# Kernel tuning notes

Hardware: AMD Instinct MI355X
Metric: run time of the kernel (lower is better)

Reference implementation:

```python
import jax, jax.numpy as jnp
import numpy as np

B = 512
DIM_X = 128
DIM_Y = 128
HIDDEN = 512


def setup_inputs() -> dict:
    key = jax.random.key(0)
    kx, ky, kw1, kw2 = jax.random.split(key, 4)
    x = jax.random.normal(kx, (B, DIM_X), dtype=jnp.float32)
    y = jax.random.normal(ky, (B, DIM_Y), dtype=jnp.float32)
    # Glorot-ish scaling for the Dense layers
    W1 = jax.random.normal(kw1, (DIM_X + DIM_Y, HIDDEN), dtype=jnp.float32) * (1.0 / np.sqrt(DIM_X + DIM_Y))
    b1 = jnp.zeros((HIDDEN,), dtype=jnp.float32)
    W2 = jax.random.normal(kw2, (HIDDEN, 1), dtype=jnp.float32) * (1.0 / np.sqrt(HIDDEN))
    b2 = jnp.zeros((1,), dtype=jnp.float32)
    return {"x": x, "y": y, "W1": W1, "b1": b1, "W2": W2, "b2": b2}


def reference(x, y, W1, b1, W2, b2):
    # scores[i, j] = f(concat(x_i, y_j)) with f = Dense(512, relu) -> Dense(1).
    # Since the first Dense is linear in the concatenated input, split W1 into
    # the x-block and y-block and broadcast-sum instead of materializing the
    # [B*B, dim_x+dim_y] concat tensor (same math as tile+concat+matmul).
    dim_x = x.shape[1]
    hx = x @ W1[:dim_x]          # [B, H]
    hy = y @ W1[dim_x:]          # [B, H]
    h = jax.nn.relu(hx[:, None, :] + hy[None, :, :] + b1)  # [B, B, H]
    scores = jnp.einsum('ijh,h->ij', h, W2[:, 0]) + b2[0]   # [B, B]
    return scores
```

## Files before the change

### kernel.cpp

```cpp
#include <hip/hip_runtime.h>


#define BATCH 512
#define DX    128
#define HID   512

typedef _Float16 half2_t __attribute__((ext_vector_type(2)));

static __device__ __forceinline__ half2_t u2h(unsigned int u) {
    union { unsigned int u; half2_t h; } c; c.u = u; return c.h;
}
static __device__ __forceinline__ unsigned int h2u(half2_t h) {
    union { half2_t h; unsigned int u; } c; c.h = h; return c.u;
}

__global__ __launch_bounds__(256) void proj_kernel(
    const float* __restrict__ x, const float* __restrict__ y,
    const float* __restrict__ W1, const float* __restrict__ b1,
    _Float16* __restrict__ hxy)
{
    const int part = blockIdx.y;
    const int row0 = blockIdx.x * 8;
    const int h0   = blockIdx.z * 256;
    const float* __restrict__ src = part ? y : x;
    const float* __restrict__ W   = W1 + part * DX * HID;

    __shared__ __align__(16) float s[8][DX];
    {
        const int t = threadIdx.x;
        const int r = t >> 5, c4 = (t & 31) << 2;
        *(float4*)&s[r][c4] = *(const float4*)&src[(row0 + r) * DX + c4];
    }
    __syncthreads();

    const int hthr = threadIdx.x & 63;
    const int rg   = threadIdx.x >> 6;
    const int h    = h0 + hthr * 4;
    const int ra   = rg * 2, rb = ra + 1;

    float a0 = 0.f, a1 = 0.f, a2 = 0.f, a3 = 0.f;
    float c0 = 0.f, c1 = 0.f, c2 = 0.f, c3 = 0.f;

    #pragma unroll 2
    for (int k4 = 0; k4 < DX / 4; ++k4) {
        const float4 xa = *(const float4*)&s[ra][k4 * 4];
        const float4 xb = *(const float4*)&s[rb][k4 * 4];
        #pragma unroll
        for (int kk = 0; kk < 4; ++kk) {
            const float4 wv = *(const float4*)&W[(k4 * 4 + kk) * HID + h];
            const float fa = (kk == 0) ? xa.x : (kk == 1) ? xa.y : (kk == 2) ? xa.z : xa.w;
            const float fb = (kk == 0) ? xb.x : (kk == 1) ? xb.y : (kk == 2) ? xb.z : xb.w;
            a0 = fmaf(fa, wv.x, a0); a1 = fmaf(fa, wv.y, a1);
            a2 = fmaf(fa, wv.z, a2); a3 = fmaf(fa, wv.w, a3);
            c0 = fmaf(fb, wv.x, c0); c1 = fmaf(fb, wv.y, c1);
            c2 = fmaf(fb, wv.z, c2); c3 = fmaf(fb, wv.w, c3);
        }
    }

    float4 bias = make_float4(0.f, 0.f, 0.f, 0.f);
    if (part) bias = *(const float4*)&b1[h];

    half2_t p0, p1;
    p0.x = (_Float16)(a0 + bias.x); p0.y = (_Float16)(a1 + bias.y);
    p1.x = (_Float16)(a2 + bias.z); p1.y = (_Float16)(a3 + bias.w);
    uint2 st0; st0.x = h2u(p0); st0.y = h2u(p1);
    *(uint2*)&hxy[(part * BATCH + row0 + ra) * HID + h] = st0;

    p0.x = (_Float16)(c0 + bias.x); p0.y = (_Float16)(c1 + bias.y);
    p1.x = (_Float16)(c2 + bias.z); p1.y = (_Float16)(c3 + bias.w);
    uint2 st1; st1.x = h2u(p0); st1.y = h2u(p1);
    *(uint2*)&hxy[(part * BATCH + row0 + rb) * HID + h] = st1;
}

#define TI   128
#define TJ   64
#define HPW  32
#define IST  132
#define JST  68

__global__ __launch_bounds__(512, 2) void score_kernel(
    const _Float16* __restrict__ hxy, const float* __restrict__ W2,
    unsigned int* __restrict__ pws16)
{
    __shared__ __align__(16) unsigned int sA[HPW * IST];
    __shared__ __align__(16) unsigned int sB[HPW * JST];
    __shared__ unsigned int sW[HPW];

    const int i0  = blockIdx.y * TI;
    const int j0  = blockIdx.x * TJ;
    const int z   = blockIdx.z;
    const int hp0 = z * HPW;
    const int tid = threadIdx.x;
    const unsigned int* __restrict__ hx32 = (const unsigned int*)hxy;

    #pragma unroll
    for (int it = 0; it < 2; ++it) {
        const int sidx = tid + it * 512;
        const int row = sidx >> 3, q = sidx & 7;
        const uint4 v = *(const uint4*)&hx32[(i0 + row) * 256 + hp0 + (q << 2)];
        unsigned int* p = &sA[(q << 2) * IST + row];
        p[0 * IST] = v.x; p[1 * IST] = v.y; p[2 * IST] = v.z; p[3 * IST] = v.w;
    }
    {
        const int row = tid >> 3, q = tid & 7;
        const uint4 v = *(const uint4*)&hx32[(BATCH + j0 + row) * 256 + hp0 + (q << 2)];
        unsigned int* p = &sB[(q << 2) * JST + row];
        p[0 * JST] = v.x; p[1 * JST] = v.y; p[2 * JST] = v.z; p[3 * JST] = v.w;
    }
    if (tid < HPW) {
        const float2 w = *(const float2*)&W2[2 * (hp0 + tid)];
        half2_t wh; wh.x = (_Float16)w.x; wh.y = (_Float16)w.y;
        sW[tid] = h2u(wh);
    }
    __syncthreads();

    const int tx = tid & 15;
    const int ty = tid >> 4;
    const unsigned int* pa = &sA[ty << 2];
    const unsigned int* pb = &sB[tx << 2];

    float acc[4][4] = {{0.f,0.f,0.f,0.f},{0.f,0.f,0.f,0.f},
                       {0.f,0.f,0.f,0.f},{0.f,0.f,0.f,0.f}};
    const half2_t hz = {(_Float16)0, (_Float16)0};

    #pragma unroll 4
    for (int hp = 0; hp < HPW; ++hp) {
        const half2_t w = u2h(sW[hp]);
        const uint4 av = *(const uint4*)&pa[hp * IST];
        const uint4 bv = *(const uint4*)&pb[hp * JST];
        half2_t a[4] = {u2h(av.x), u2h(av.y), u2h(av.z), u2h(av.w)};
        half2_t b[4] = {u2h(bv.x), u2h(bv.y), u2h(bv.z), u2h(bv.w)};
        #pragma unroll
        for (int r = 0; r < 4; ++r)
            #pragma unroll
            for (int c = 0; c < 4; ++c) {
                half2_t t = a[r] + b[c];
                t = __builtin_elementwise_max(t, hz);
                acc[r][c] = __builtin_amdgcn_fdot2(t, w, acc[r][c], false);
            }
    }

    const int i = i0 + (ty << 2);
    unsigned int* dst = pws16 + z * (BATCH * BATCH / 2);
    #pragma unroll
    for (int r = 0; r < 4; ++r) {
        half2_t p0, p1;
        p0.x = (_Float16)acc[r][0]; p0.y = (_Float16)acc[r][1];
        p1.x = (_Float16)acc[r][2]; p1.y = (_Float16)acc[r][3];
        uint2 st; st.x = h2u(p0); st.y = h2u(p1);
        *(uint2*)&dst[(i + r) * (BATCH / 2) + (j0 >> 1) + (tx << 1)] = st;
    }
}

__global__ __launch_bounds__(256) void reduce_kernel(
    const uint2* __restrict__ pws16, const float* __restrict__ b2,
    float* __restrict__ out)
{
    const int gid = blockIdx.x * 256 + threadIdx.x;
    float s0 = 0.f, s1 = 0.f, s2 = 0.f, s3 = 0.f;
    #pragma unroll
    for (int zz = 0; zz < 8; ++zz) {
        const uint2 v = pws16[zz * (BATCH * BATCH / 4) + gid];
        const half2_t hA = u2h(v.x), hB = u2h(v.y);
        s0 += (float)hA.x; s1 += (float)hA.y;
        s2 += (float)hB.x; s3 += (float)hB.y;
    }
    const float bs = b2[0];
    *(float4*)&out[gid * 4] = make_float4(s0 + bs, s1 + bs, s2 + bs, s3 + bs);
}

extern "C" void kernel_launch(void* const* d_in, const int* in_sizes, int n_in,
                              void* d_out, int out_size, void* d_ws, size_t ws_size,
                              hipStream_t stream) {
    const float* x  = (const float*)d_in[0];
    const float* y  = (const float*)d_in[1];
    const float* W1 = (const float*)d_in[2];
    const float* b1 = (const float*)d_in[3];
    const float* W2 = (const float*)d_in[4];
    const float* b2 = (const float*)d_in[5];
    float* out = (float*)d_out;

    _Float16* hxy       = (_Float16*)d_ws;
    unsigned int* pws16 = (unsigned int*)((char*)d_ws + (1 << 20));

    proj_kernel<<<dim3(BATCH / 8, 2, 2), 256, 0, stream>>>(x, y, W1, b1, hxy);
    score_kernel<<<dim3(BATCH / TJ, BATCH / TI, 8), 512, 0, stream>>>(hxy, W2, pws16);
    reduce_kernel<<<dim3(256), 256, 0, stream>>>((const uint2*)pws16, b2, out);
}
```

Baseline: 86.09 us.

## Fuse split-H reduction into score kernel via per-wave shared-memory partials

The score kernel now gives each block a 32x32 output tile covering the full hidden dimension. Each of its 8 waves handles a 32-wide slice of H, and the partial sums are reduced through shared memory inside the block. This removes the separate reduce kernel, one launch, and the global fp16 partial-sum round trip. The cost is smaller output tiles, so each block reloads more A/B data from global memory relative to the outputs it produces. Shared memory per block rises to about 90KB, which may lower occupancy.

```diff
diff --git a/kernel.cpp b/kernel.cpp
--- a/kernel.cpp
+++ b/kernel.cpp
@@ -72,50 +72,52 @@
     *(uint2*)&hxy[(part * BATCH + row0 + rb) * HID + h] = st1;
 }
 
-#define TI   128
-#define TJ   64
-#define HPW  32
-#define IST  132
-#define JST  68
+#define TI   32
+#define TJ   32
+#define AST  36
+#define PST  17
 
-__global__ __launch_bounds__(512, 2) void score_kernel(
+__global__ __launch_bounds__(512) void score_kernel(
     const _Float16* __restrict__ hxy, const float* __restrict__ W2,
-    unsigned int* __restrict__ pws16)
+    const float* __restrict__ b2, float* __restrict__ out)
 {
-    __shared__ __align__(16) unsigned int sA[HPW * IST];
-    __shared__ __align__(16) unsigned int sB[HPW * JST];
-    __shared__ unsigned int sW[HPW];
+    __shared__ __align__(16) unsigned int sA[256 * AST];
+    __shared__ __align__(16) unsigned int sB[256 * AST];
+    __shared__ unsigned int sW[256];
+    __shared__ unsigned int pP[8][TI * PST];
 
     const int i0  = blockIdx.y * TI;
     const int j0  = blockIdx.x * TJ;
-    const int z   = blockIdx.z;
-    const int hp0 = z * HPW;
     const int tid = threadIdx.x;
     const unsigned int* __restrict__ hx32 = (const unsigned int*)hxy;
 
     #pragma unroll
-    for (int it = 0; it < 2; ++it) {
-        const int sidx = tid + it * 512;
-        const int row = sidx >> 3, q = sidx & 7;
-        const uint4 v = *(const uint4*)&hx32[(i0 + row) * 256 + hp0 + (q << 2)];
-        unsigned int* p = &sA[(q << 2) * IST + row];
-        p[0 * IST] = v.x; p[1 * IST] = v.y; p[2 * IST] = v.z; p[3 * IST] = v.w;
+    for (int it = 0; it < 4; ++it) {
+        const int sidx  = tid + it * 512;
+        const int q8    = sidx & 7;
+        const int row   = (sidx >> 3) & 31;
+        const int chunk = sidx >> 8;
+        const int q     = chunk * 8 + q8;
+        const uint4 va = *(const uint4*)&hx32[(i0 + row) * 256 + (q << 2)];
+        unsigned int* pa = &sA[(q << 2) * AST + row];
+        pa[0 * AST] = va.x; pa[1 * AST] = va.y; pa[2 * AST] = va.z; pa[3 * AST] = va.w;
+        const uint4 vb = *(const uint4*)&hx32[(BATCH + j0 + row) * 256 + (q << 2)];
+        unsigned int* pb = &sB[(q << 2) * AST + row];
+        pb[0 * AST] = vb.x; pb[1 * AST] = vb.y; pb[2 * AST] = vb.z; pb[3 * AST] = vb.w;
     }
-    {
-        const int row = tid >> 3, q = tid & 7;
-        const uint4 v = *(const uint4*)&hx32[(BATCH + j0 + row) * 256 + hp0 + (q << 2)];
-        unsigned int* p = &sB[(q << 2) * JST + row];
-        p[0 * JST] = v.x; p[1 * JST] = v.y; p[2 * JST] = v.z; p[3 * JST] = v.w;
-    }
-    if (tid < HPW) {
-        const float2 w = *(const float2*)&W2[2 * (hp0 + tid)];
+    if (tid < 256) {
+        const float2 w = *(const float2*)&W2[2 * tid];
         half2_t wh; wh.x = (_Float16)w.x; wh.y = (_Float16)w.y;
         sW[tid] = h2u(wh);
     }
     __syncthreads();
 
-    const int tx = tid & 15;
-    const int ty = tid >> 4;
+    const int wave = tid >> 6;
+    const int lane = tid & 63;
+    const int tx   = lane & 7;
+    const int ty   = lane >> 3;
+    const int hp0  = wave * 32;
+
     const unsigned int* pa = &sA[ty << 2];
     const unsigned int* pb = &sB[tx << 2];
 
@@ -124,10 +126,11 @@
     const half2_t hz = {(_Float16)0, (_Float16)0};
 
     #pragma unroll 4
-    for (int hp = 0; hp < HPW; ++hp) {
+    for (int hpl = 0; hpl < 32; ++hpl) {
+        const int hp = hp0 + hpl;
         const half2_t w = u2h(sW[hp]);
-        const uint4 av = *(const uint4*)&pa[hp * IST];
-        const uint4 bv = *(const uint4*)&pb[hp * JST];
+        const uint4 av = *(const uint4*)&pa[hp * AST];
+        const uint4 bv = *(const uint4*)&pb[hp * AST];
         half2_t a[4] = {u2h(av.x), u2h(av.y), u2h(av.z), u2h(av.w)};
         half2_t b[4] = {u2h(bv.x), u2h(bv.y), u2h(bv.z), u2h(bv.w)};
         #pragma unroll
@@ -140,33 +143,33 @@
             }
     }
 
-    const int i = i0 + (ty << 2);
-    unsigned int* dst = pws16 + z * (BATCH * BATCH / 2);
-    #pragma unroll
-    for (int r = 0; r < 4; ++r) {
-        half2_t p0, p1;
-        p0.x = (_Float16)acc[r][0]; p0.y = (_Float16)acc[r][1];
-        p1.x = (_Float16)acc[r][2]; p1.y = (_Float16)acc[r][3];
-        uint2 st; st.x = h2u(p0); st.y = h2u(p1);
-        *(uint2*)&dst[(i + r) * (BATCH / 2) + (j0 >> 1) + (tx << 1)] = st;
+    {
+        unsigned int* pz = &pP[wave][0];
+        #pragma unroll
+        for (int r = 0; r < 4; ++r) {
+            half2_t p0, p1;
+            p0.x = (_Float16)acc[r][0]; p0.y = (_Float16)acc[r][1];
+            p1.x = (_Float16)acc[r][2]; p1.y = (_Float16)acc[r][3];
+            const int irow = (ty << 2) + r;
+            pz[irow * PST + (tx << 1)]     = h2u(p0);
+            pz[irow * PST + (tx << 1) + 1] = h2u(p1);
+        }
     }
-}
+    __syncthreads();
 
-__global__ __launch_bounds__(256) void reduce_kernel(
-    const uint2* __restrict__ pws16, const float* __restrict__ b2,
-    float* __restrict__ out)
-{
-    const int gid = blockIdx.x * 256 + threadIdx.x;
-    float s0 = 0.f, s1 = 0.f, s2 = 0.f, s3 = 0.f;
-    #pragma unroll
-    for (int zz = 0; zz < 8; ++zz) {
-        const uint2 v = pws16[zz * (BATCH * BATCH / 4) + gid];
-        const half2_t hA = u2h(v.x), hB = u2h(v.y);
-        s0 += (float)hA.x; s1 += (float)hA.y;
-        s2 += (float)hB.x; s3 += (float)hB.y;
+    {
+        const int i  = tid >> 4;
+        const int jp = tid & 15;
+        float s0 = 0.f, s1 = 0.f;
+        #pragma unroll
+        for (int z = 0; z < 8; ++z) {
+            const half2_t v = u2h(pP[z][i * PST + jp]);
+            s0 += (float)v.x; s1 += (float)v.y;
+        }
+        const float bs = b2[0];
+        *(float2*)&out[(i0 + i) * BATCH + j0 + (jp << 1)] =
+            make_float2(s0 + bs, s1 + bs);
     }
-    const float bs = b2[0];
-    *(float4*)&out[gid * 4] = make_float4(s0 + bs, s1 + bs, s2 + bs, s3 + bs);
 }
 
 extern "C" void kernel_launch(void* const* d_in, const int* in_sizes, int n_in,
@@ -180,10 +183,8 @@
     const float* b2 = (const float*)d_in[5];
     float* out = (float*)d_out;
 
-    _Float16* hxy       = (_Float16*)d_ws;
-    unsigned int* pws16 = (unsigned int*)((char*)d_ws + (1 << 20));
+    _Float16* hxy = (_Float16*)d_ws;
 
     proj_kernel<<<dim3(BATCH / 8, 2, 2), 256, 0, stream>>>(x, y, W1, b1, hxy);
-    score_kernel<<<dim3(BATCH / TJ, BATCH / TI, 8), 512, 0, stream>>>(hxy, W2, pws16);
-    reduce_kernel<<<dim3(256), 256, 0, stream>>>((const uint2*)pws16, b2, out);
+    score_kernel<<<dim3(BATCH / TJ, BATCH / TI), 512, 0, stream>>>(hxy, W2, b2, out);
 }
```

After: 81.87 us. -4.9%, faster.
